# Kernel tuning notes

Measured on AMD Instinct MI355X. Metric: run time of the kernel, lower is better.

The kernel has to match this reference:

```python
import jax, jax.numpy as jnp
import numpy as np

B, T, E, H, D = 2, 2048, 1024, 16, 64
ROPE_BASE = 10000.0


def project(x, k):
    # Lift to Lorentz hyperboloid with curvature magnitude K=exp(k): <lx,lx>_L = -K
    K = jnp.exp(k)
    x0 = jnp.sqrt(K + jnp.sum(x * x, axis=-1, keepdims=True))
    return jnp.concatenate([x0, x], axis=-1)


def layer_norm(x, w, b, eps=1e-5):
    m = jnp.mean(x, axis=-1, keepdims=True)
    v = jnp.mean((x - m) ** 2, axis=-1, keepdims=True)
    return (x - m) * jax.lax.rsqrt(v + eps) * w + b


def setup_inputs() -> dict:
    key = jax.random.key(0)
    ks = jax.random.split(key, 8)
    s = 0.02
    return dict(
        x=jax.random.normal(ks[0], (B, T, E), jnp.float32),
        block_curvature=jnp.asarray(1.0, jnp.float32),
        mlp_curvature=jnp.asarray(1.0, jnp.float32),
        attn_curvatures=jnp.ones((1, H, 1, 1), jnp.float32),
        w_qkv=jax.random.normal(ks[1], (E + 1, 3 * E), jnp.float32) * s,
        w_attn_proj=jax.random.normal(ks[2], ((D + 1) * H, E), jnp.float32) * s,
        b_attn_proj=jnp.zeros((E,), jnp.float32),
        w_mlp_expand=jax.random.normal(ks[3], (E + 1, 4 * E + 3), jnp.float32) * s,
        b_mlp_expand=jnp.zeros((4 * E + 3,), jnp.float32),
        w_mlp_shrink=jax.random.normal(ks[4], (4 * (E + 1), E), jnp.float32) * s,
        b_mlp_shrink=jnp.zeros((E,), jnp.float32),
        ln_w=jnp.ones((E,), jnp.float32),
        ln_b=jnp.zeros((E,), jnp.float32),
    )


def _block(x, block_curvature, mlp_curvature, attn_curvatures, w_qkv,
           w_attn_proj, b_attn_proj, w_mlp_expand, b_mlp_expand,
           w_mlp_shrink, b_mlp_shrink, ln_w, ln_b):
    Bq, Tq = x.shape[0], x.shape[1]
    lx = project(x, block_curvature)  # (B,T,E+1)

    def block_norm(l):
        return project(layer_norm(l[..., 1:], ln_w, ln_b), block_curvature)

    def skip(l, f):  # hyperbolic skip: add space parts, re-lift
        return project(l[..., 1:] + f[..., 1:], block_curvature)

    def attn(l):
        qkv = l @ w_qkv  # (B,T,3E)
        q, k, v = jnp.split(qkv, 3, axis=-1)
        q = q.reshape(Bq, Tq, H, D)
        k = k.reshape(Bq, Tq, H, D)
        v = v.reshape(Bq, Tq, H, D)
        half = D // 2
        inv_freq = 1.0 / (ROPE_BASE ** (jnp.arange(0, D, 2, dtype=jnp.float32) / D))
        freqs = jnp.arange(Tq, dtype=jnp.float32)[:, None] * inv_freq[None, :]
        cos = jnp.cos(freqs)[None, :, None, :]  # (1,T,1,D/2)
        sin = jnp.sin(freqs)[None, :, None, :]

        def rope(t):
            t1, t2 = t[..., :half], t[..., half:]
            return jnp.concatenate([t1 * cos + t2 * sin, -t1 * sin + t2 * cos], axis=-1)

        q = rope(q).transpose(0, 2, 1, 3)  # (B,H,T,D)
        k = rope(k).transpose(0, 2, 1, 3)
        v = v.transpose(0, 2, 1, 3)
        K = jnp.exp(attn_curvatures)  # (1,H,1,1) per-head curvature
        qt = jnp.sqrt(K + jnp.sum(q * q, axis=-1, keepdims=True))  # time coord (B,H,T,1)
        kt = jnp.sqrt(K + jnp.sum(k * k, axis=-1, keepdims=True))
        lv = project(v, attn_curvatures)  # (B,H,T,D+1)
        # Lorentz inner product without materializing (B,H,T,T,D+1)
        inner = jnp.einsum('bhtd,bhsd->bhts', q, k) - qt * jnp.swapaxes(kt, -1, -2)
        ratio = jnp.maximum(-inner / K, 1.0 + 1e-7)
        dis = jnp.sqrt(K) * jnp.arccosh(ratio)  # (B,H,T,T)
        causal = jnp.tril(jnp.ones((Tq, Tq), dtype=bool))
        w = jnp.where(causal, -dis, -jnp.inf)  # neg_dis attention weight + causal bias
        aw = jax.nn.softmax(w, axis=-1)
        o = jnp.einsum('bhts,bhse->bhte', aw, lv)  # (B,H,T,D+1)
        lnorm2 = o[..., :1] ** 2 - jnp.sum(o[..., 1:] ** 2, axis=-1, keepdims=True)
        hn = jnp.sqrt(jnp.maximum(lnorm2, 1e-12))  # Lorentz norm
        o = o * jnp.sqrt(K) / hn  # renormalize back onto hyperboloid
        o = o.transpose(0, 2, 1, 3).reshape(Bq, Tq, H * (D + 1))
        return project(o @ w_attn_proj + b_attn_proj, block_curvature)

    def mlp(l):
        h = project(l @ w_mlp_expand + b_mlp_expand, mlp_curvature)[..., 1:]  # (B,T,4E+3)
        h = jax.nn.gelu(h, approximate=False)
        h = project(h, mlp_curvature)  # (B,T,4(E+1))
        return project(h @ w_mlp_shrink + b_mlp_shrink, block_curvature)

    lx = skip(lx, attn(block_norm(lx)))
    lx = skip(lx, mlp(block_norm(lx)))
    return lx


def reference(x, block_curvature, mlp_curvature, attn_curvatures, w_qkv,
              w_attn_proj, b_attn_proj, w_mlp_expand, b_mlp_expand,
              w_mlp_shrink, b_mlp_shrink, ln_w, ln_b):
    return _block(x, block_curvature, mlp_curvature, attn_curvatures, w_qkv,
                  w_attn_proj, b_attn_proj, w_mlp_expand, b_mlp_expand,
                  w_mlp_shrink, b_mlp_shrink, ln_w, ln_b)
```

## Files before the change

kernel.cpp:

```cpp
#include <hip/hip_runtime.h>
#include <math.h>

#define MM   4096
#define TT   2048
#define HH   16

typedef __bf16 bf16x8 __attribute__((ext_vector_type(8)));
typedef float f32x4 __attribute__((ext_vector_type(4)));

__device__ __forceinline__ void g2l16(const void* g, void* l) {
    __builtin_amdgcn_global_load_lds(
        (__attribute__((address_space(1))) void*)g,
        (__attribute__((address_space(3))) void*)l, 16, 0, 0);
}

#if __has_builtin(__builtin_amdgcn_exp2f)
__device__ __forceinline__ float fexp2(float x) { return __builtin_amdgcn_exp2f(x); }
#else
__device__ __forceinline__ float fexp2(float x) { return exp2f(x); }
#endif
#if __has_builtin(__builtin_amdgcn_logf)
__device__ __forceinline__ float flog2(float x) { return __builtin_amdgcn_logf(x); }
#else
__device__ __forceinline__ float flog2(float x) { return log2f(x); }
#endif
#if __has_builtin(__builtin_amdgcn_sqrtf)
__device__ __forceinline__ float fsqrt_(float x) { return __builtin_amdgcn_sqrtf(x); }
#else
__device__ __forceinline__ float fsqrt_(float x) { return sqrtf(x); }
#endif
#if __has_builtin(__builtin_amdgcn_rcpf)
__device__ __forceinline__ float frcp_(float x) { return __builtin_amdgcn_rcpf(x); }
#else
__device__ __forceinline__ float frcp_(float x) { return 1.0f / x; }
#endif
#if __has_builtin(__builtin_amdgcn_rsqf)
__device__ __forceinline__ float frsq_(float x) { return __builtin_amdgcn_rsqf(x); }
#else
__device__ __forceinline__ float frsq_(float x) { return rsqrtf(x); }
#endif

__device__ __forceinline__ float gelu_f(float x) {
    float u = 0.7978845608028654f * fmaf(0.044715f * x, x * x, x);
    u = fminf(fmaxf(u, -15.f), 15.f);
    float t = fexp2(-2.885390081777927f * u);
    return 0.5f * x * (1.f + (1.f - t) * frcp_(1.f + t));
}

__device__ __forceinline__ float blockSum256(float v, volatile float* sb) {
    int lane = threadIdx.x & 63, w = threadIdx.x >> 6;
#pragma unroll
    for (int o = 32; o; o >>= 1) v += __shfl_xor(v, o);
    if (lane == 0) sb[w] = v;
    __syncthreads();
    v = sb[0] + sb[1] + sb[2] + sb[3];
    __syncthreads();
    return v;
}

__global__ __launch_bounds__(256) void block_norm_bf_k(
    const float* __restrict__ in, int ld,
    __bf16* __restrict__ out, int ldo,
    const float* __restrict__ lw, const float* __restrict__ lb,
    const float* __restrict__ curv)
{
    int row = blockIdx.x;
    const float* x = in + (size_t)row * ld;
    __bf16* o = out + (size_t)row * ldo;
    __shared__ float sb[4];
    int tid = threadIdx.x;
    float v[4]; float s1 = 0.f, s2 = 0.f;
#pragma unroll
    for (int r = 0; r < 4; r++) {
        float t = x[tid + 256 * r];
        v[r] = t; s1 += t; s2 += t * t;
    }
    s1 = blockSum256(s1, sb);
    s2 = blockSum256(s2, sb);
    float mean = s1 * (1.f / 1024.f);
    float var  = s2 * (1.f / 1024.f) - mean * mean;
    float rs = rsqrtf(var + 1e-5f);
    float y[4]; float ssq = 0.f;
#pragma unroll
    for (int r = 0; r < 4; r++) {
        int i = tid + 256 * r;
        float t = (v[r] - mean) * rs * lw[i] + lb[i];
        y[r] = t; ssq += t * t;
    }
    ssq = blockSum256(ssq, sb);
#pragma unroll
    for (int r = 0; r < 4; r++) o[1 + tid + 256 * r] = (__bf16)y[r];
    if (tid == 0) o[0] = (__bf16)sqrtf(expf(*curv) + ssq);
    if (tid < ldo - 1025) o[1025 + tid] = (__bf16)0.f;
}

__global__ __launch_bounds__(256) void row_x0_k(
    float* __restrict__ buf, int stride, int n, const float* __restrict__ curv)
{
    int row = blockIdx.x;
    float* base = buf + (size_t)row * stride;
    __shared__ float sb[4];
    float s = 0.f;
    for (int i = threadIdx.x; i < n; i += 256) { float t = base[1 + i]; s += t * t; }
    s = blockSum256(s, sb);
    if (threadIdx.x == 0) base[0] = sqrtf(expf(*curv) + s);
}

__global__ __launch_bounds__(256) void row_x0_tail_k(
    __bf16* __restrict__ h,
    const __bf16* __restrict__ ln,
    const __bf16* __restrict__ Bt,
    const float* __restrict__ bias,
    const float* __restrict__ curv)
{
    int row = blockIdx.x;
    __bf16* base = h + (size_t)row * 4224;
    const __bf16* lnr = ln + (size_t)row * 1088;
    const __bf16* B0 = Bt + (size_t)4096 * 1088;
    const __bf16* B1 = Bt + (size_t)4097 * 1088;
    const __bf16* B2 = Bt + (size_t)4098 * 1088;
    __shared__ float sb[4];
    float d0 = 0.f, d1 = 0.f, d2 = 0.f;
    for (int i = threadIdx.x; i < 1088; i += 256) {
        float a = (float)lnr[i];
        d0 += a * (float)B0[i];
        d1 += a * (float)B1[i];
        d2 += a * (float)B2[i];
    }
    d0 = blockSum256(d0, sb);
    d1 = blockSum256(d1, sb);
    d2 = blockSum256(d2, sb);
    float t3[3] = {d0 + bias[4096], d1 + bias[4097], d2 + bias[4098]};
    float ssq_t = 0.f;
#pragma unroll
    for (int j = 0; j < 3; j++) {
        float v = gelu_f(t3[j]);
        t3[j] = v; ssq_t += v * v;
    }
    if (threadIdx.x == 0) {
        base[1 + 4096] = (__bf16)t3[0];
        base[1 + 4097] = (__bf16)t3[1];
        base[1 + 4098] = (__bf16)t3[2];
    }
    float s = 0.f;
    for (int i = threadIdx.x; i < 4096; i += 256) { float t = (float)base[1 + i]; s += t * t; }
    s = blockSum256(s, sb) + ssq_t;
    if (threadIdx.x == 0) base[0] = (__bf16)sqrtf(expf(*curv) + s);
    if (threadIdx.x < 124) base[4100 + threadIdx.x] = (__bf16)0.f;
}

__global__ __launch_bounds__(256) void wt_k(
    const float* __restrict__ W, int K, int N,
    __bf16* __restrict__ Wt, int Kp)
{
    __shared__ float s[32][33];
    int tx = threadIdx.x & 31, ty = threadIdx.x >> 5;
    int k0 = blockIdx.x * 32, n0 = blockIdx.y * 32;
#pragma unroll
    for (int r = 0; r < 4; r++) {
        int k = k0 + ty + 8 * r, n = n0 + tx;
        s[ty + 8 * r][tx] = (k < K && n < N) ? W[(size_t)k * N + n] : 0.f;
    }
    __syncthreads();
#pragma unroll
    for (int r = 0; r < 4; r++) {
        int n = n0 + ty + 8 * r, k = k0 + tx;
        if (n < N) Wt[(size_t)n * Kp + k] = (__bf16)s[tx][ty + 8 * r];
    }
}

template<bool BIAS, bool GELU, bool OUTBF>
__global__ __launch_bounds__(512, 2) void mgemm256_k(
    const __bf16* __restrict__ A, int lda,
    const __bf16* __restrict__ Bt, int ldb, int NB,
    const float* __restrict__ bias,
    void* __restrict__ Cout, int ldc,
    int N, int Kp)
{
    __shared__ __bf16 sAB[65536];
    const int tid = threadIdx.x;
    const int w = tid >> 6, lane = tid & 63;
    const int wm = w >> 2, wn = w & 3;
    const int lr = lane & 15, lq = lane >> 4;

    const int lin = blockIdx.y * gridDim.x + blockIdx.x;
    const int xcd = lin & 7, loc = lin >> 3;
    const int LN = gridDim.x >> 1, LM = gridDim.y >> 2;
    const int mt = (xcd >> 1) * LM + loc / LN;
    const int nt = (xcd & 1) * LN + loc % LN;
    const int m0 = mt * 256, n0 = nt * 256;

    const int rr  = tid >> 3;
    const int csw = ((tid & 7) ^ (rr & 7)) << 3;
    const __bf16* gA[4]; const __bf16* gB[4];
#pragma unroll
    for (int c = 0; c < 4; c++) {
        gA[c] = A + (size_t)(m0 + c * 64 + rr) * lda + csw;
        int rb = n0 + c * 64 + rr; rb = (rb < NB) ? rb : (NB - 1);
        gB[c] = Bt + (size_t)rb * ldb + csw;
    }
    __bf16* lA = sAB + (w << 9);
    __bf16* lB = sAB + 32768 + (w << 9);

    const int off0 = (lq * 8) ^ ((lr & 7) << 3);
    const int off1 = off0 ^ 32;
    const int arow = wm * 128 + lr;
    const int brow = wn * 64 + lr;

    f32x4 zero = {0.f, 0.f, 0.f, 0.f};
    f32x4 acc[8][4];
#pragma unroll
    for (int i = 0; i < 8; i++)
#pragma unroll
        for (int j = 0; j < 4; j++) acc[i][j] = zero;

#pragma unroll
    for (int c = 0; c < 4; c++) {
        g2l16(gA[c], lA + c * 4096);
        g2l16(gB[c], lB + c * 4096);
    }
    asm volatile("s_waitcnt vmcnt(0)" ::: "memory");
    __builtin_amdgcn_s_barrier();

    const int NT = Kp >> 6;
    for (int kt = 0; kt < NT; ++kt) {
        const int cur = kt & 1;
        const __bf16* pA = sAB + cur * 16384;
        const __bf16* pB = sAB + 32768 + cur * 16384;
        bf16x8 af[4][2], bfr[4][2];

        if (kt + 1 < NT) {
            const int ko = (kt + 1) << 6;
            __bf16* dA = lA + (cur ^ 1) * 16384;
            __bf16* dB = lB + (cur ^ 1) * 16384;
#pragma unroll
            for (int c = 0; c < 4; c++) {
                g2l16(gA[c] + ko, dA + c * 4096);
                g2l16(gB[c] + ko, dB + c * 4096);
            }
        }
#pragma unroll
        for (int i = 0; i < 4; i++) {
            const __bf16* r = pA + (arow + i * 16) * 64;
            af[i][0] = *(const bf16x8*)(r + off0);
            af[i][1] = *(const bf16x8*)(r + off1);
        }
#pragma unroll
        for (int j = 0; j < 2; j++) {
            const __bf16* r = pB + (brow + j * 16) * 64;
            bfr[j][0] = *(const bf16x8*)(r + off0);
            bfr[j][1] = *(const bf16x8*)(r + off1);
        }
        __builtin_amdgcn_s_barrier();
        __builtin_amdgcn_s_setprio(1);
#pragma unroll
        for (int ks = 0; ks < 2; ks++)
#pragma unroll
            for (int i = 0; i < 4; i++)
#pragma unroll
                for (int j = 0; j < 2; j++)
                    acc[i][j] = __builtin_amdgcn_mfma_f32_16x16x32_bf16(af[i][ks], bfr[j][ks], acc[i][j], 0, 0, 0);
        __builtin_amdgcn_s_setprio(0);
        __builtin_amdgcn_s_barrier();

#pragma unroll
        for (int j = 2; j < 4; j++) {
            const __bf16* r = pB + (brow + j * 16) * 64;
            bfr[j][0] = *(const bf16x8*)(r + off0);
            bfr[j][1] = *(const bf16x8*)(r + off1);
        }
        __builtin_amdgcn_s_barrier();
        __builtin_amdgcn_s_setprio(1);
#pragma unroll
        for (int ks = 0; ks < 2; ks++)
#pragma unroll
            for (int i = 0; i < 4; i++)
#pragma unroll
                for (int j = 2; j < 4; j++)
                    acc[i][j] = __builtin_amdgcn_mfma_f32_16x16x32_bf16(af[i][ks], bfr[j][ks], acc[i][j], 0, 0, 0);
        __builtin_amdgcn_s_setprio(0);
        __builtin_amdgcn_s_barrier();

#pragma unroll
        for (int i = 0; i < 4; i++) {
            const __bf16* r = pA + (arow + 64 + i * 16) * 64;
            af[i][0] = *(const bf16x8*)(r + off0);
            af[i][1] = *(const bf16x8*)(r + off1);
        }
        __builtin_amdgcn_s_barrier();
        __builtin_amdgcn_s_setprio(1);
#pragma unroll
        for (int ks = 0; ks < 2; ks++)
#pragma unroll
            for (int i = 0; i < 4; i++)
#pragma unroll
                for (int j = 0; j < 2; j++)
                    acc[4 + i][j] = __builtin_amdgcn_mfma_f32_16x16x32_bf16(af[i][ks], bfr[j][ks], acc[4 + i][j], 0, 0, 0);
        __builtin_amdgcn_s_setprio(0);
        __builtin_amdgcn_s_barrier();

        __builtin_amdgcn_s_setprio(1);
#pragma unroll
        for (int ks = 0; ks < 2; ks++)
#pragma unroll
            for (int i = 0; i < 4; i++)
#pragma unroll
                for (int j = 2; j < 4; j++)
                    acc[4 + i][j] = __builtin_amdgcn_mfma_f32_16x16x32_bf16(af[i][ks], bfr[j][ks], acc[4 + i][j], 0, 0, 0);
        __builtin_amdgcn_s_setprio(0);
        asm volatile("s_waitcnt vmcnt(0) lgkmcnt(0)" ::: "memory");
        __builtin_amdgcn_s_barrier();
    }

#pragma unroll
    for (int j = 0; j < 4; j++) {
        const int n = n0 + wn * 64 + j * 16 + lr;
        if (n < N) {
            const float bv = BIAS ? bias[n] : 0.f;
#pragma unroll
            for (int i = 0; i < 8; i++) {
#pragma unroll
                for (int r = 0; r < 4; r++) {
                    const int m = m0 + wm * 128 + i * 16 + lq * 4 + r;
                    float v = acc[i][j][r] + bv;
                    if (GELU) v = gelu_f(v);
                    if (OUTBF) ((__bf16*)Cout)[(size_t)m * ldc + n] = (__bf16)v;
                    else       ((float*)Cout)[(size_t)m * ldc + n] = v;
                }
            }
        }
    }
}

template<bool BIAS, bool GELU, bool SKIP>
__global__ __launch_bounds__(256, 2) void mgemm128_k(
    const __bf16* __restrict__ A, int lda,
    const __bf16* __restrict__ Bt, int ldb,
    const float* __restrict__ bias,
    const float* __restrict__ skip, int ldskip,
    float* __restrict__ Cout, int ldc,
    int N, int Kp)
{
    __shared__ __bf16 sAB[32768];
    const int tid = threadIdx.x;
    const int w = tid >> 6, lane = tid & 63;
    const int wm = w >> 1, wn = w & 1;
    const int lr = lane & 15, lq = lane >> 4;

    const int bid = blockIdx.x;
    const int cpx = gridDim.x >> 3;
    const int swz = (bid & 7) * cpx + (bid >> 3);
    const int m0 = (swz >> 3) * 128, n0 = (swz & 7) * 128;

    const int rr  = tid >> 3;
    const int csw = ((tid & 7) ^ (rr & 7)) << 3;
    const __bf16* gA[4]; const __bf16* gB[4];
#pragma unroll
    for (int c = 0; c < 4; c++) {
        gA[c] = A + (size_t)(m0 + c * 32 + rr) * lda + csw;
        gB[c] = Bt + (size_t)(n0 + c * 32 + rr) * ldb + csw;
    }
    __bf16* lA = sAB + (w << 9);
    __bf16* lB = sAB + 16384 + (w << 9);

    const int off0 = (lq * 8) ^ ((lr & 7) << 3);
    const int off1 = off0 ^ 32;
    const int arow = wm * 64 + lr;
    const int brow = wn * 64 + lr;

    f32x4 zero = {0.f, 0.f, 0.f, 0.f};
    f32x4 acc[4][4];
#pragma unroll
    for (int i = 0; i < 4; i++)
#pragma unroll
        for (int j = 0; j < 4; j++) acc[i][j] = zero;

#pragma unroll
    for (int c = 0; c < 4; c++) {
        g2l16(gA[c], lA + c * 2048);
        g2l16(gB[c], lB + c * 2048);
    }
    asm volatile("s_waitcnt vmcnt(0)" ::: "memory");
    __builtin_amdgcn_s_barrier();

    const int NT = Kp >> 6;
    for (int kt = 0; kt < NT; ++kt) {
        const int cur = kt & 1;
        const __bf16* pA = sAB + cur * 8192;
        const __bf16* pB = sAB + 16384 + cur * 8192;
        bf16x8 af[4][2], bfr[4][2];

        if (kt + 1 < NT) {
            const int ko = (kt + 1) << 6;
            __bf16* dA = lA + (cur ^ 1) * 8192;
            __bf16* dB = lB + (cur ^ 1) * 8192;
#pragma unroll
            for (int c = 0; c < 4; c++) {
                g2l16(gA[c] + ko, dA + c * 2048);
                g2l16(gB[c] + ko, dB + c * 2048);
            }
        }
#pragma unroll
        for (int i = 0; i < 4; i++) {
            const __bf16* r = pA + (arow + i * 16) * 64;
            af[i][0] = *(const bf16x8*)(r + off0);
            af[i][1] = *(const bf16x8*)(r + off1);
        }
#pragma unroll
        for (int j = 0; j < 2; j++) {
            const __bf16* r = pB + (brow + j * 16) * 64;
            bfr[j][0] = *(const bf16x8*)(r + off0);
            bfr[j][1] = *(const bf16x8*)(r + off1);
        }
        __builtin_amdgcn_s_barrier();
        __builtin_amdgcn_s_setprio(1);
#pragma unroll
        for (int ks = 0; ks < 2; ks++)
#pragma unroll
            for (int i = 0; i < 4; i++)
#pragma unroll
                for (int j = 0; j < 2; j++)
                    acc[i][j] = __builtin_amdgcn_mfma_f32_16x16x32_bf16(af[i][ks], bfr[j][ks], acc[i][j], 0, 0, 0);
        __builtin_amdgcn_s_setprio(0);
        __builtin_amdgcn_s_barrier();

#pragma unroll
        for (int j = 2; j < 4; j++) {
            const __bf16* r = pB + (brow + j * 16) * 64;
            bfr[j][0] = *(const bf16x8*)(r + off0);
            bfr[j][1] = *(const bf16x8*)(r + off1);
        }
        __builtin_amdgcn_s_barrier();
        __builtin_amdgcn_s_setprio(1);
#pragma unroll
        for (int ks = 0; ks < 2; ks++)
#pragma unroll
            for (int i = 0; i < 4; i++)
#pragma unroll
                for (int j = 2; j < 4; j++)
                    acc[i][j] = __builtin_amdgcn_mfma_f32_16x16x32_bf16(af[i][ks], bfr[j][ks], acc[i][j], 0, 0, 0);
        __builtin_amdgcn_s_setprio(0);
        asm volatile("s_waitcnt vmcnt(0) lgkmcnt(0)" ::: "memory");
        __builtin_amdgcn_s_barrier();
    }

#pragma unroll
    for (int j = 0; j < 4; j++) {
        const int n = n0 + wn * 64 + j * 16 + lr;
        if (n < N) {
            const float bv = BIAS ? bias[n] : 0.f;
#pragma unroll
            for (int i = 0; i < 4; i++) {
#pragma unroll
                for (int r = 0; r < 4; r++) {
                    const int m = m0 + wm * 64 + i * 16 + lq * 4 + r;
                    float v = acc[i][j][r] + bv;
                    if (GELU) v = gelu_f(v);
                    if (SKIP) v += skip[(size_t)m * ldskip + n];
                    Cout[(size_t)m * ldc + n] = v;
                }
            }
        }
    }
}

__global__ __launch_bounds__(256) void rope_k(
    float* __restrict__ QKV, const float* __restrict__ curv,
    float* __restrict__ qt, float* __restrict__ kt,
    __bf16* __restrict__ Kb, __bf16* __restrict__ Obf)
{
    int row = blockIdx.x;
    int b = row >> 11, t = row & (TT - 1);
    int wv = threadIdx.x >> 6, d = threadIdx.x & 63;
    int j = d & 31;
    float fr = (float)t * powf(10000.0f, -(float)(2 * j) / 64.0f);
    float cv = cosf(fr), sv = sinf(fr);
    float sgn = (d < 32) ? sv : -sv;
    for (int h = wv; h < HH; h += 4) {
        float Kh = expf(curv[h]);
        float* base = QKV + (size_t)row * 3072 + h * 64;
        float q = base[d], k = base[1024 + d];
        float qp = __shfl_xor(q, 32);
        float kp = __shfl_xor(k, 32);
        float qr = q * cv + qp * sgn;
        float kr = k * cv + kp * sgn;
        base[d] = qr;
        size_t oidx = ((size_t)(b * HH + h) * TT + t);
        Kb[oidx * 64 + d] = (__bf16)kr;
        float sq = qr * qr, sk = kr * kr;
#pragma unroll
        for (int o = 32; o; o >>= 1) {
            sq += __shfl_xor(sq, o);
            sk += __shfl_xor(sk, o);
        }
        if (d == 0) {
            qt[oidx] = sqrtf(Kh + sq);
            kt[oidx] = sqrtf(Kh + sk);
        }
    }
    if (threadIdx.x < 48) Obf[(size_t)row * 1088 + 1040 + threadIdx.x] = (__bf16)0.f;
}

__global__ __launch_bounds__(256) void vtrans_k(
    const float* __restrict__ QKV, const float* __restrict__ curv,
    __bf16* __restrict__ Vtb, float* __restrict__ vt)
{
    __shared__ float sT[64 * 65];
    int bh = blockIdx.y; int h = bh & (HH - 1); int b = bh >> 4;
    int t0 = blockIdx.x * 64;
    int tid = threadIdx.x, w = tid >> 6, lane = tid & 63;
    float Kh = expf(curv[h]);
    const float* vbase = QKV + (size_t)(b * TT + t0) * 3072 + 2048 + h * 64;
#pragma unroll 4
    for (int i = 0; i < 16; i++) {
        int tr = w * 16 + i;
        float v = vbase[(size_t)tr * 3072 + lane];
        sT[lane * 65 + tr] = v;
        float s = v * v;
#pragma unroll
        for (int o = 32; o; o >>= 1) s += __shfl_xor(s, o);
        if (lane == 0) vt[(size_t)bh * TT + t0 + tr] = sqrtf(Kh + s);
    }
    __syncthreads();
    int d = tid >> 2, seg = tid & 3;
    const float* r = &sT[d * 65 + seg * 16];
    bf16x8 o0, o1;
#pragma unroll
    for (int i = 0; i < 8; i++) { o0[i] = (__bf16)r[i]; o1[i] = (__bf16)r[8 + i]; }
    __bf16* dst = Vtb + ((size_t)bh * 64 + d) * TT + t0 + seg * 16;
    *(bf16x8*)dst = o0;
    *(bf16x8*)(dst + 8) = o1;
}

__global__ __launch_bounds__(256, 3) void flash_k(
    const float* __restrict__ QKV,
    const __bf16* __restrict__ Kb, const __bf16* __restrict__ Vtb,
    const float* __restrict__ qt, const float* __restrict__ kt,
    const float* __restrict__ vt,
    const float* __restrict__ curv,
    __bf16* __restrict__ O)
{
    __shared__ __bf16 sK[2][4096];
    __shared__ __bf16 sVt[2][4096];
    __shared__ __bf16 sP[4 * 16 * 72];
    __shared__ float skt[2][64], svt[2][64];

    int bh = blockIdx.x; int h = bh & (HH - 1); int b = bh >> 4;
    int qti = 31 - (int)blockIdx.y;
    int q0 = qti << 6;
    int NJ = qti + 1;
    float Kh = expf(curv[h]);
    float sqKh = sqrtf(Kh), msqK = -sqKh, invKh = 1.0f / Kh;
    const float* tok = QKV + (size_t)b * TT * 3072 + h * 64;
    const char* KbB = (const char*)Kb + (size_t)bh * TT * 128;
    const char* VtB = (const char*)Vtb + (size_t)bh * 64 * (TT * 2);
    const float* qtp = qt + (size_t)bh * TT;
    const float* ktp = kt + (size_t)bh * TT;
    const float* vtp = vt + (size_t)bh * TT;

    int tid = threadIdx.x;
    int w = tid >> 6, lane = tid & 63;
    int m = lane & 15, quad = lane >> 4;
    int myBase = q0 + 16 * w;
    __bf16* sPw = &sP[w * 16 * 72];

    bf16x8 qhi[2], qlo[2];
    {
        const float* qrow = tok + (size_t)(myBase + m) * 3072;
#pragma unroll
        for (int ks = 0; ks < 2; ks++) {
            const float* s = qrow + quad * 8 + 32 * ks;
            float4 f0 = *(const float4*)s;
            float4 f1 = *(const float4*)(s + 4);
            float fa[8] = {f0.x, f0.y, f0.z, f0.w, f1.x, f1.y, f1.z, f1.w};
#pragma unroll
            for (int jj = 0; jj < 8; jj++) {
                __bf16 hv = (__bf16)fa[jj];
                qhi[ks][jj] = hv;
                qlo[ks][jj] = (__bf16)(fa[jj] - (float)hv);
            }
        }
    }
    float qtv[4]; int qg[4];
#pragma unroll
    for (int r = 0; r < 4; r++) { qg[r] = myBase + quad * 4 + r; qtv[r] = qtp[qg[r]]; }

    f32x4 zero = {0.f, 0.f, 0.f, 0.f};
    f32x4 accO[4];
#pragma unroll
    for (int nt = 0; nt < 4; nt++) accO[nt] = zero;
    float lsumr[4] = {}, o0r[4] = {};

    {
        const char* kg = KbB + (size_t)lane * 128 + w * 16;
        char* sKb = (char*)&sK[0][0] + w * 1024;
        g2l16(kg,      sKb);
        g2l16(kg + 64, sKb + 4096);
        const char* vg = VtB + (size_t)lane * (TT * 2) + w * 16;
        char* sVb = (char*)&sVt[0][0] + w * 1024;
        g2l16(vg,      sVb);
        g2l16(vg + 64, sVb + 4096);
    }
    if (tid < 64) skt[0][tid] = ktp[tid];
    else if (tid < 128) svt[0][tid - 64] = vtp[tid - 64];
    __syncthreads();

    for (int j = 0; j < NJ; ++j) {
        int cur = j & 1;
        int sb = j << 6;
        if (j + 1 < NJ) {
            int sb2 = sb + 64;
            const char* kg = KbB + (size_t)(sb2 + lane) * 128 + w * 16;
            char* sKb = (char*)&sK[cur ^ 1][0] + w * 1024;
            g2l16(kg,      sKb);
            g2l16(kg + 64, sKb + 4096);
            const char* vg = VtB + (size_t)lane * (TT * 2) + sb2 * 2 + w * 16;
            char* sVb = (char*)&sVt[cur ^ 1][0] + w * 1024;
            g2l16(vg,      sVb);
            g2l16(vg + 64, sVb + 4096);
            if (tid < 64) skt[cur ^ 1][tid] = ktp[sb2 + tid];
            else if (tid < 128) svt[cur ^ 1][tid - 64] = vtp[sb2 + tid - 64];
        }

        f32x4 accS[4];
#pragma unroll
        for (int nt = 0; nt < 4; nt++) accS[nt] = zero;
#pragma unroll
        for (int nt = 0; nt < 4; nt++) {
#pragma unroll
            for (int ksp = 0; ksp < 2; ksp++) {
                bf16x8 bk = *(const bf16x8*)&sK[cur][((ksp * 4 + quad) * 64 + nt * 16 + m) * 8];
                accS[nt] = __builtin_amdgcn_mfma_f32_16x16x32_bf16(qhi[ksp], bk, accS[nt], 0, 0, 0);
                accS[nt] = __builtin_amdgcn_mfma_f32_16x16x32_bf16(qlo[ksp], bk, accS[nt], 0, 0, 0);
            }
        }
#pragma unroll
        for (int nt = 0; nt < 4; nt++) {
            int col = nt * 16 + m;
            int sglob = sb + col;
            float ktv = skt[cur][col], vtv = svt[cur][col];
#pragma unroll
            for (int r = 0; r < 4; r++) {
                float dot = accS[nt][r];
                float rdiff = fmaf(qtv[r], ktv, -dot);
                float ratio = fmaxf(rdiff * invKh, 1.0f + 1e-7f);
                float y = ratio + fsqrt_(fmaf(ratio, ratio, -1.0f));
                float pv = fexp2(msqK * flog2(y));
                float p = (sglob <= qg[r]) ? pv : 0.0f;
                lsumr[r] += p;
                o0r[r] = fmaf(p, vtv, o0r[r]);
                sPw[(quad * 4 + r) * 72 + col] = (__bf16)p;
            }
        }
        __asm__ volatile("s_waitcnt lgkmcnt(0)" ::: "memory");
#pragma unroll
        for (int ksp = 0; ksp < 2; ksp++) {
            bf16x8 aP = *(const bf16x8*)&sPw[m * 72 + ksp * 32 + quad * 8];
#pragma unroll
            for (int nt = 0; nt < 4; nt++) {
                bf16x8 bV = *(const bf16x8*)&sVt[cur][((ksp * 4 + quad) * 64 + nt * 16 + m) * 8];
                accO[nt] = __builtin_amdgcn_mfma_f32_16x16x32_bf16(aP, bV, accO[nt], 0, 0, 0);
            }
        }
        __syncthreads();
    }

#pragma unroll
    for (int r = 0; r < 4; r++) {
#pragma unroll
        for (int off = 1; off < 16; off <<= 1) {
            lsumr[r] += __shfl_xor(lsumr[r], off);
            o0r[r]   += __shfl_xor(o0r[r], off);
        }
    }
#pragma unroll
    for (int r = 0; r < 4; r++) {
        float inv = frcp_(lsumr[r]);
        float o0f = o0r[r] * inv;
        float ov[4]; float part = 0.f;
#pragma unroll
        for (int nt = 0; nt < 4; nt++) { float t = accO[nt][r] * inv; ov[nt] = t; part += t * t; }
        part += __shfl_xor(part, 1);
        part += __shfl_xor(part, 2);
        part += __shfl_xor(part, 4);
        part += __shfl_xor(part, 8);
        float scale = sqKh * frsq_(fmaxf(o0f * o0f - part, 1e-12f));
        size_t orow = (size_t)(b * TT + qg[r]) * 1088 + h * 65;
        if (m == 0) O[orow] = (__bf16)(o0f * scale);
#pragma unroll
        for (int nt = 0; nt < 4; nt++) O[orow + 1 + nt * 16 + m] = (__bf16)(ov[nt] * scale);
    }
}

extern "C" void kernel_launch(void* const* d_in, const int* in_sizes, int n_in,
                              void* d_out, int out_size, void* d_ws, size_t ws_size,
                              hipStream_t stream) {
    const float* x    = (const float*)d_in[0];
    const float* bc   = (const float*)d_in[1];
    const float* mc   = (const float*)d_in[2];
    const float* ac   = (const float*)d_in[3];
    const float* w_qkv = (const float*)d_in[4];
    const float* w_ap  = (const float*)d_in[5];
    const float* b_ap  = (const float*)d_in[6];
    const float* w_me  = (const float*)d_in[7];
    const float* b_me  = (const float*)d_in[8];
    const float* w_ms  = (const float*)d_in[9];
    const float* b_ms  = (const float*)d_in[10];
    const float* lnw  = (const float*)d_in[11];
    const float* lnb  = (const float*)d_in[12];
    float* out = (float*)d_out;
    float* ws  = (float*)d_ws;

    float* R      = ws;
    float* qkvbuf = R;
    float* X2     = R;
    __bf16* h_bf  = (__bf16*)(R + 4194304);
    float* p      = R + 12845056;
    __bf16* ln_bf = (__bf16*)p;  p += 2228224;
    __bf16* o_bf  = (__bf16*)p;  p += 2228224;
    __bf16* qkvT  = (__bf16*)p;  p += 1671168;
    __bf16* apT   = (__bf16*)p;  p += 557056;
    float*  meT_f = p;           p += 2229856;
    float*  msT_f = p;           p += 2162688;
    float* Qt = p;               p += 2 * HH * TT;
    float* Kt = p;               p += 2 * HH * TT;
    float* Vt = p;
    __bf16* meT = (__bf16*)meT_f;
    __bf16* msT = (__bf16*)msT_f;
    __bf16* Kb  = (__bf16*)meT_f;
    __bf16* Vtb = (__bf16*)msT_f;

    wt_k<<<dim3(34, 96),  256, 0, stream>>>(w_qkv, 1025, 3072, qkvT, 1088);
    wt_k<<<dim3(34, 32),  256, 0, stream>>>(w_ap,  1040, 1024, apT,  1088);

    block_norm_bf_k<<<MM, 256, 0, stream>>>(x, 1024, ln_bf, 1088, lnw, lnb, bc);
    mgemm256_k<false, false, false><<<dim3(12, 16), 512, 0, stream>>>(
        ln_bf, 1088, qkvT, 1088, 3072, nullptr, qkvbuf, 3072, 3072, 1088);
    rope_k<<<MM, 256, 0, stream>>>(qkvbuf, ac, Qt, Kt, Kb, o_bf);
    vtrans_k<<<dim3(32, 32), 256, 0, stream>>>(qkvbuf, ac, Vtb, Vt);
    flash_k<<<dim3(2 * HH, 32), 256, 0, stream>>>(qkvbuf, Kb, Vtb, Qt, Kt, Vt, ac, o_bf);
    wt_k<<<dim3(34, 129), 256, 0, stream>>>(w_me,  1025, 4099, meT, 1088);
    wt_k<<<dim3(132, 32), 256, 0, stream>>>(w_ms,  4100, 1024, msT, 4224);
    mgemm128_k<true, false, true><<<dim3(256), 256, 0, stream>>>(
        o_bf, 1088, apT, 1088, b_ap, x, 1024, X2, 1024, 1024, 1088);
    block_norm_bf_k<<<MM, 256, 0, stream>>>(X2, 1024, ln_bf, 1088, lnw, lnb, bc);
    mgemm256_k<true, true, true><<<dim3(16, 16), 512, 0, stream>>>(
        ln_bf, 1088, meT, 1088, 4099, b_me, (void*)(h_bf + 1), 4224, 4099, 1088);
    row_x0_tail_k<<<MM, 256, 0, stream>>>(h_bf, ln_bf, meT, b_me, mc);
    mgemm128_k<true, false, true><<<dim3(256), 256, 0, stream>>>(
        h_bf, 4224, msT, 4224, b_ms, X2, 1024, out + 1, 1025, 1024, 4224);
    row_x0_k<<<MM, 256, 0, stream>>>(out, 1025, 1024, bc);
}
```

Baseline: 444.4 us.

## Enlarge flash query tile to 128 rows and use 128-tile GEMM for QKV

The flash attention kernel now runs 8 waves per block over 128 query rows, up from 4 waves over 64. Each K/V tile loaded into LDS is therefore reused by twice as many query rows, and each thread issues one async load per tile. MFMA sections are wrapped in s_setprio so matrix work gets issue priority over the softmax ALU code. The QKV projection moves from the 256-tile GEMM to the 128-tile GEMM, which gains a configurable N-tile count, to launch more blocks. The risks are more register and LDS pressure per block and coarser causal work balance across blocks.

```diff
diff --git a/kernel.cpp b/kernel.cpp
--- a/kernel.cpp
+++ b/kernel.cpp
@@ -339,7 +339,7 @@
     const float* __restrict__ bias,
     const float* __restrict__ skip, int ldskip,
     float* __restrict__ Cout, int ldc,
-    int N, int Kp)
+    int N, int Kp, int nT)
 {
     __shared__ __bf16 sAB[32768];
     const int tid = threadIdx.x;
@@ -350,7 +350,7 @@
     const int bid = blockIdx.x;
     const int cpx = gridDim.x >> 3;
     const int swz = (bid & 7) * cpx + (bid >> 3);
-    const int m0 = (swz >> 3) * 128, n0 = (swz & 7) * 128;
+    const int m0 = (swz / nT) * 128, n0 = (swz % nT) * 128;
 
     const int rr  = tid >> 3;
     const int csw = ((tid & 7) ^ (rr & 7)) << 3;
@@ -532,7 +532,7 @@
     *(bf16x8*)(dst + 8) = o1;
 }
 
-__global__ __launch_bounds__(256, 3) void flash_k(
+__global__ __launch_bounds__(512, 4) void flash_k(
     const float* __restrict__ QKV,
     const __bf16* __restrict__ Kb, const __bf16* __restrict__ Vtb,
     const float* __restrict__ qt, const float* __restrict__ kt,
@@ -542,13 +542,13 @@
 {
     __shared__ __bf16 sK[2][4096];
     __shared__ __bf16 sVt[2][4096];
-    __shared__ __bf16 sP[4 * 16 * 72];
+    __shared__ __bf16 sP[8 * 16 * 72];
     __shared__ float skt[2][64], svt[2][64];
 
     int bh = blockIdx.x; int h = bh & (HH - 1); int b = bh >> 4;
-    int qti = 31 - (int)blockIdx.y;
-    int q0 = qti << 6;
-    int NJ = qti + 1;
+    int qti = 15 - (int)blockIdx.y;
+    int q0 = qti << 7;
+    int NJ = (qti << 1) + 2;
     float Kh = expf(curv[h]);
     float sqKh = sqrtf(Kh), msqK = -sqKh, invKh = 1.0f / Kh;
     const float* tok = QKV + (size_t)b * TT * 3072 + h * 64;
@@ -561,6 +561,7 @@
     int tid = threadIdx.x;
     int w = tid >> 6, lane = tid & 63;
     int m = lane & 15, quad = lane >> 4;
+    int wq = w & 3, half = w >> 2;
     int myBase = q0 + 16 * w;
     __bf16* sPw = &sP[w * 16 * 72];
 
@@ -591,16 +592,10 @@
     for (int nt = 0; nt < 4; nt++) accO[nt] = zero;
     float lsumr[4] = {}, o0r[4] = {};
 
-    {
-        const char* kg = KbB + (size_t)lane * 128 + w * 16;
-        char* sKb = (char*)&sK[0][0] + w * 1024;
-        g2l16(kg,      sKb);
-        g2l16(kg + 64, sKb + 4096);
-        const char* vg = VtB + (size_t)lane * (TT * 2) + w * 16;
-        char* sVb = (char*)&sVt[0][0] + w * 1024;
-        g2l16(vg,      sVb);
-        g2l16(vg + 64, sVb + 4096);
-    }
+    const int stoff = half * 4096 + wq * 1024;
+
+    g2l16(KbB + (size_t)lane * 128 + half * 64 + wq * 16, (char*)&sK[0][0] + stoff);
+    g2l16(VtB + (size_t)lane * (TT * 2) + half * 64 + wq * 16, (char*)&sVt[0][0] + stoff);
     if (tid < 64) skt[0][tid] = ktp[tid];
     else if (tid < 128) svt[0][tid - 64] = vtp[tid - 64];
     __syncthreads();
@@ -610,14 +605,10 @@
         int sb = j << 6;
         if (j + 1 < NJ) {
             int sb2 = sb + 64;
-            const char* kg = KbB + (size_t)(sb2 + lane) * 128 + w * 16;
-            char* sKb = (char*)&sK[cur ^ 1][0] + w * 1024;
-            g2l16(kg,      sKb);
-            g2l16(kg + 64, sKb + 4096);
-            const char* vg = VtB + (size_t)lane * (TT * 2) + sb2 * 2 + w * 16;
-            char* sVb = (char*)&sVt[cur ^ 1][0] + w * 1024;
-            g2l16(vg,      sVb);
-            g2l16(vg + 64, sVb + 4096);
+            g2l16(KbB + (size_t)(sb2 + lane) * 128 + half * 64 + wq * 16,
+                  (char*)&sK[cur ^ 1][0] + stoff);
+            g2l16(VtB + (size_t)lane * (TT * 2) + sb2 * 2 + half * 64 + wq * 16,
+                  (char*)&sVt[cur ^ 1][0] + stoff);
             if (tid < 64) skt[cur ^ 1][tid] = ktp[sb2 + tid];
             else if (tid < 128) svt[cur ^ 1][tid - 64] = vtp[sb2 + tid - 64];
         }
@@ -625,6 +616,7 @@
         f32x4 accS[4];
 #pragma unroll
         for (int nt = 0; nt < 4; nt++) accS[nt] = zero;
+        __builtin_amdgcn_s_setprio(1);
 #pragma unroll
         for (int nt = 0; nt < 4; nt++) {
 #pragma unroll
@@ -634,6 +626,7 @@
                 accS[nt] = __builtin_amdgcn_mfma_f32_16x16x32_bf16(qlo[ksp], bk, accS[nt], 0, 0, 0);
             }
         }
+        __builtin_amdgcn_s_setprio(0);
 #pragma unroll
         for (int nt = 0; nt < 4; nt++) {
             int col = nt * 16 + m;
@@ -653,6 +646,7 @@
             }
         }
         __asm__ volatile("s_waitcnt lgkmcnt(0)" ::: "memory");
+        __builtin_amdgcn_s_setprio(1);
 #pragma unroll
         for (int ksp = 0; ksp < 2; ksp++) {
             bf16x8 aP = *(const bf16x8*)&sPw[m * 72 + ksp * 32 + quad * 8];
@@ -662,6 +656,7 @@
                 accO[nt] = __builtin_amdgcn_mfma_f32_16x16x32_bf16(aP, bV, accO[nt], 0, 0, 0);
             }
         }
+        __builtin_amdgcn_s_setprio(0);
         __syncthreads();
     }
 
@@ -734,20 +729,20 @@
     wt_k<<<dim3(34, 32),  256, 0, stream>>>(w_ap,  1040, 1024, apT,  1088);
 
     block_norm_bf_k<<<MM, 256, 0, stream>>>(x, 1024, ln_bf, 1088, lnw, lnb, bc);
-    mgemm256_k<false, false, false><<<dim3(12, 16), 512, 0, stream>>>(
-        ln_bf, 1088, qkvT, 1088, 3072, nullptr, qkvbuf, 3072, 3072, 1088);
+    mgemm128_k<false, false, false><<<dim3(768), 256, 0, stream>>>(
+        ln_bf, 1088, qkvT, 1088, nullptr, nullptr, 0, qkvbuf, 3072, 3072, 1088, 24);
     rope_k<<<MM, 256, 0, stream>>>(qkvbuf, ac, Qt, Kt, Kb, o_bf);
     vtrans_k<<<dim3(32, 32), 256, 0, stream>>>(qkvbuf, ac, Vtb, Vt);
-    flash_k<<<dim3(2 * HH, 32), 256, 0, stream>>>(qkvbuf, Kb, Vtb, Qt, Kt, Vt, ac, o_bf);
+    flash_k<<<dim3(2 * HH, 16), 512, 0, stream>>>(qkvbuf, Kb, Vtb, Qt, Kt, Vt, ac, o_bf);
     wt_k<<<dim3(34, 129), 256, 0, stream>>>(w_me,  1025, 4099, meT, 1088);
     wt_k<<<dim3(132, 32), 256, 0, stream>>>(w_ms,  4100, 1024, msT, 4224);
     mgemm128_k<true, false, true><<<dim3(256), 256, 0, stream>>>(
-        o_bf, 1088, apT, 1088, b_ap, x, 1024, X2, 1024, 1024, 1088);
+        o_bf, 1088, apT, 1088, b_ap, x, 1024, X2, 1024, 1024, 1088, 8);
     block_norm_bf_k<<<MM, 256, 0, stream>>>(X2, 1024, ln_bf, 1088, lnw, lnb, bc);
     mgemm256_k<true, true, true><<<dim3(16, 16), 512, 0, stream>>>(
         ln_bf, 1088, meT, 1088, 4099, b_me, (void*)(h_bf + 1), 4224, 4099, 1088);
     row_x0_tail_k<<<MM, 256, 0, stream>>>(h_bf, ln_bf, meT, b_me, mc);
     mgemm128_k<true, false, true><<<dim3(256), 256, 0, stream>>>(
-        h_bf, 4224, msT, 4224, b_ms, X2, 1024, out + 1, 1025, 1024, 4224);
+        h_bf, 4224, msT, 4224, b_ms, X2, 1024, out + 1, 1025, 1024, 4224, 8);
     row_x0_k<<<MM, 256, 0, stream>>>(out, 1025, 1024, bc);
 }
```

After: 463.3 us. +4.2%, slower.

## Replace 256-tile GEMM with a 3-stage, BK=32, 128-tile GEMM for all projections

Applied to the files above, without the earlier changes.

Drops the 512-thread 256x256 GEMM kernel and routes the QKV and MLP-expand GEMMs through a reworked 128x128 kernel. That kernel now uses a K-step of 32, a three-buffer global-to-LDS pipeline with partial vmcnt waits, a new swizzle, and launch bounds of 3 blocks per CU. A bf16-output template flag is added so it can also serve the expand GEMM. The aim is more blocks in flight and deeper prefetch, traded against lower per-tile data reuse. The expand GEMM now computes only 4096 columns, which relies on the tail kernel covering the remaining ones.

```diff
diff --git a/kernel.cpp b/kernel.cpp
--- a/kernel.cpp
+++ b/kernel.cpp
@@ -169,179 +169,16 @@
     }
 }
 
-template<bool BIAS, bool GELU, bool OUTBF>
-__global__ __launch_bounds__(512, 2) void mgemm256_k(
-    const __bf16* __restrict__ A, int lda,
-    const __bf16* __restrict__ Bt, int ldb, int NB,
-    const float* __restrict__ bias,
-    void* __restrict__ Cout, int ldc,
-    int N, int Kp)
-{
-    __shared__ __bf16 sAB[65536];
-    const int tid = threadIdx.x;
-    const int w = tid >> 6, lane = tid & 63;
-    const int wm = w >> 2, wn = w & 3;
-    const int lr = lane & 15, lq = lane >> 4;
-
-    const int lin = blockIdx.y * gridDim.x + blockIdx.x;
-    const int xcd = lin & 7, loc = lin >> 3;
-    const int LN = gridDim.x >> 1, LM = gridDim.y >> 2;
-    const int mt = (xcd >> 1) * LM + loc / LN;
-    const int nt = (xcd & 1) * LN + loc % LN;
-    const int m0 = mt * 256, n0 = nt * 256;
-
-    const int rr  = tid >> 3;
-    const int csw = ((tid & 7) ^ (rr & 7)) << 3;
-    const __bf16* gA[4]; const __bf16* gB[4];
-#pragma unroll
-    for (int c = 0; c < 4; c++) {
-        gA[c] = A + (size_t)(m0 + c * 64 + rr) * lda + csw;
-        int rb = n0 + c * 64 + rr; rb = (rb < NB) ? rb : (NB - 1);
-        gB[c] = Bt + (size_t)rb * ldb + csw;
-    }
-    __bf16* lA = sAB + (w << 9);
-    __bf16* lB = sAB + 32768 + (w << 9);
-
-    const int off0 = (lq * 8) ^ ((lr & 7) << 3);
-    const int off1 = off0 ^ 32;
-    const int arow = wm * 128 + lr;
-    const int brow = wn * 64 + lr;
-
-    f32x4 zero = {0.f, 0.f, 0.f, 0.f};
-    f32x4 acc[8][4];
-#pragma unroll
-    for (int i = 0; i < 8; i++)
-#pragma unroll
-        for (int j = 0; j < 4; j++) acc[i][j] = zero;
-
-#pragma unroll
-    for (int c = 0; c < 4; c++) {
-        g2l16(gA[c], lA + c * 4096);
-        g2l16(gB[c], lB + c * 4096);
-    }
-    asm volatile("s_waitcnt vmcnt(0)" ::: "memory");
-    __builtin_amdgcn_s_barrier();
-
-    const int NT = Kp >> 6;
-    for (int kt = 0; kt < NT; ++kt) {
-        const int cur = kt & 1;
-        const __bf16* pA = sAB + cur * 16384;
-        const __bf16* pB = sAB + 32768 + cur * 16384;
-        bf16x8 af[4][2], bfr[4][2];
-
-        if (kt + 1 < NT) {
-            const int ko = (kt + 1) << 6;
-            __bf16* dA = lA + (cur ^ 1) * 16384;
-            __bf16* dB = lB + (cur ^ 1) * 16384;
-#pragma unroll
-            for (int c = 0; c < 4; c++) {
-                g2l16(gA[c] + ko, dA + c * 4096);
-                g2l16(gB[c] + ko, dB + c * 4096);
-            }
-        }
-#pragma unroll
-        for (int i = 0; i < 4; i++) {
-            const __bf16* r = pA + (arow + i * 16) * 64;
-            af[i][0] = *(const bf16x8*)(r + off0);
-            af[i][1] = *(const bf16x8*)(r + off1);
-        }
-#pragma unroll
-        for (int j = 0; j < 2; j++) {
-            const __bf16* r = pB + (brow + j * 16) * 64;
-            bfr[j][0] = *(const bf16x8*)(r + off0);
-            bfr[j][1] = *(const bf16x8*)(r + off1);
-        }
-        __builtin_amdgcn_s_barrier();
-        __builtin_amdgcn_s_setprio(1);
-#pragma unroll
-        for (int ks = 0; ks < 2; ks++)
-#pragma unroll
-            for (int i = 0; i < 4; i++)
-#pragma unroll
-                for (int j = 0; j < 2; j++)
-                    acc[i][j] = __builtin_amdgcn_mfma_f32_16x16x32_bf16(af[i][ks], bfr[j][ks], acc[i][j], 0, 0, 0);
-        __builtin_amdgcn_s_setprio(0);
-        __builtin_amdgcn_s_barrier();
-
-#pragma unroll
-        for (int j = 2; j < 4; j++) {
-            const __bf16* r = pB + (brow + j * 16) * 64;
-            bfr[j][0] = *(const bf16x8*)(r + off0);
-            bfr[j][1] = *(const bf16x8*)(r + off1);
-        }
-        __builtin_amdgcn_s_barrier();
-        __builtin_amdgcn_s_setprio(1);
-#pragma unroll
-        for (int ks = 0; ks < 2; ks++)
-#pragma unroll
-            for (int i = 0; i < 4; i++)
-#pragma unroll
-                for (int j = 2; j < 4; j++)
-                    acc[i][j] = __builtin_amdgcn_mfma_f32_16x16x32_bf16(af[i][ks], bfr[j][ks], acc[i][j], 0, 0, 0);
-        __builtin_amdgcn_s_setprio(0);
-        __builtin_amdgcn_s_barrier();
-
-#pragma unroll
-        for (int i = 0; i < 4; i++) {
-            const __bf16* r = pA + (arow + 64 + i * 16) * 64;
-            af[i][0] = *(const bf16x8*)(r + off0);
-            af[i][1] = *(const bf16x8*)(r + off1);
-        }
-        __builtin_amdgcn_s_barrier();
-        __builtin_amdgcn_s_setprio(1);
-#pragma unroll
-        for (int ks = 0; ks < 2; ks++)
-#pragma unroll
-            for (int i = 0; i < 4; i++)
-#pragma unroll
-                for (int j = 0; j < 2; j++)
-                    acc[4 + i][j] = __builtin_amdgcn_mfma_f32_16x16x32_bf16(af[i][ks], bfr[j][ks], acc[4 + i][j], 0, 0, 0);
-        __builtin_amdgcn_s_setprio(0);
-        __builtin_amdgcn_s_barrier();
-
-        __builtin_amdgcn_s_setprio(1);
-#pragma unroll
-        for (int ks = 0; ks < 2; ks++)
-#pragma unroll
-            for (int i = 0; i < 4; i++)
-#pragma unroll
-                for (int j = 2; j < 4; j++)
-                    acc[4 + i][j] = __builtin_amdgcn_mfma_f32_16x16x32_bf16(af[i][ks], bfr[j][ks], acc[4 + i][j], 0, 0, 0);
-        __builtin_amdgcn_s_setprio(0);
-        asm volatile("s_waitcnt vmcnt(0) lgkmcnt(0)" ::: "memory");
-        __builtin_amdgcn_s_barrier();
-    }
-
-#pragma unroll
-    for (int j = 0; j < 4; j++) {
-        const int n = n0 + wn * 64 + j * 16 + lr;
-        if (n < N) {
-            const float bv = BIAS ? bias[n] : 0.f;
-#pragma unroll
-            for (int i = 0; i < 8; i++) {
-#pragma unroll
-                for (int r = 0; r < 4; r++) {
-                    const int m = m0 + wm * 128 + i * 16 + lq * 4 + r;
-                    float v = acc[i][j][r] + bv;
-                    if (GELU) v = gelu_f(v);
-                    if (OUTBF) ((__bf16*)Cout)[(size_t)m * ldc + n] = (__bf16)v;
-                    else       ((float*)Cout)[(size_t)m * ldc + n] = v;
-                }
-            }
-        }
-    }
-}
-
-template<bool BIAS, bool GELU, bool SKIP>
-__global__ __launch_bounds__(256, 2) void mgemm128_k(
+template<bool BIAS, bool GELU, bool SKIP, bool OUTBF>
+__global__ __launch_bounds__(256, 3) void mgemm128_k(
     const __bf16* __restrict__ A, int lda,
     const __bf16* __restrict__ Bt, int ldb,
     const float* __restrict__ bias,
     const float* __restrict__ skip, int ldskip,
-    float* __restrict__ Cout, int ldc,
-    int N, int Kp)
-{
-    __shared__ __bf16 sAB[32768];
+    void* __restrict__ Cout, int ldc,
+    int N, int Kp, int nT)
+{
+    __shared__ __bf16 sAB[24576];
     const int tid = threadIdx.x;
     const int w = tid >> 6, lane = tid & 63;
     const int wm = w >> 1, wn = w & 1;
@@ -350,21 +187,19 @@
     const int bid = blockIdx.x;
     const int cpx = gridDim.x >> 3;
     const int swz = (bid & 7) * cpx + (bid >> 3);
-    const int m0 = (swz >> 3) * 128, n0 = (swz & 7) * 128;
-
-    const int rr  = tid >> 3;
-    const int csw = ((tid & 7) ^ (rr & 7)) << 3;
-    const __bf16* gA[4]; const __bf16* gB[4];
-#pragma unroll
-    for (int c = 0; c < 4; c++) {
-        gA[c] = A + (size_t)(m0 + c * 32 + rr) * lda + csw;
-        gB[c] = Bt + (size_t)(n0 + c * 32 + rr) * ldb + csw;
-    }
-    __bf16* lA = sAB + (w << 9);
-    __bf16* lB = sAB + 16384 + (w << 9);
-
-    const int off0 = (lq * 8) ^ ((lr & 7) << 3);
-    const int off1 = off0 ^ 32;
+    const int m0 = (swz / nT) * 128, n0 = (swz % nT) * 128;
+
+    const int rr  = tid >> 2;
+    const int csw = ((tid & 3) ^ ((rr >> 1) & 3)) << 3;
+    const __bf16* gA[2]; const __bf16* gB[2];
+#pragma unroll
+    for (int c = 0; c < 2; c++) {
+        gA[c] = A + (size_t)(m0 + c * 64 + rr) * lda + csw;
+        gB[c] = Bt + (size_t)(n0 + c * 64 + rr) * ldb + csw;
+    }
+    const int wst = w * 512;
+
+    const int off = (lq ^ ((lr >> 1) & 3)) << 3;
     const int arow = wm * 64 + lr;
     const int brow = wn * 64 + lr;
 
@@ -375,73 +210,49 @@
 #pragma unroll
         for (int j = 0; j < 4; j++) acc[i][j] = zero;
 
-#pragma unroll
-    for (int c = 0; c < 4; c++) {
-        g2l16(gA[c], lA + c * 2048);
-        g2l16(gB[c], lB + c * 2048);
-    }
-    asm volatile("s_waitcnt vmcnt(0)" ::: "memory");
+    const int NT = Kp >> 5;
+#pragma unroll
+    for (int c = 0; c < 2; c++) {
+        g2l16(gA[c], sAB + c * 2048 + wst);
+        g2l16(gB[c], sAB + 12288 + c * 2048 + wst);
+    }
+#pragma unroll
+    for (int c = 0; c < 2; c++) {
+        g2l16(gA[c] + 32, sAB + 4096 + c * 2048 + wst);
+        g2l16(gB[c] + 32, sAB + 12288 + 4096 + c * 2048 + wst);
+    }
+    asm volatile("s_waitcnt vmcnt(4)" ::: "memory");
     __builtin_amdgcn_s_barrier();
 
-    const int NT = Kp >> 6;
+    int cur = 0;
     for (int kt = 0; kt < NT; ++kt) {
-        const int cur = kt & 1;
-        const __bf16* pA = sAB + cur * 8192;
-        const __bf16* pB = sAB + 16384 + cur * 8192;
-        bf16x8 af[4][2], bfr[4][2];
-
-        if (kt + 1 < NT) {
-            const int ko = (kt + 1) << 6;
-            __bf16* dA = lA + (cur ^ 1) * 8192;
-            __bf16* dB = lB + (cur ^ 1) * 8192;
-#pragma unroll
-            for (int c = 0; c < 4; c++) {
-                g2l16(gA[c] + ko, dA + c * 2048);
-                g2l16(gB[c] + ko, dB + c * 2048);
+        if (kt + 2 < NT) {
+            const int sbuf = (cur == 0) ? 2 : (cur - 1);
+            const int ko = (kt + 2) << 5;
+#pragma unroll
+            for (int c = 0; c < 2; c++) {
+                g2l16(gA[c] + ko, sAB + sbuf * 4096 + c * 2048 + wst);
+                g2l16(gB[c] + ko, sAB + 12288 + sbuf * 4096 + c * 2048 + wst);
             }
         }
-#pragma unroll
-        for (int i = 0; i < 4; i++) {
-            const __bf16* r = pA + (arow + i * 16) * 64;
-            af[i][0] = *(const bf16x8*)(r + off0);
-            af[i][1] = *(const bf16x8*)(r + off1);
-        }
-#pragma unroll
-        for (int j = 0; j < 2; j++) {
-            const __bf16* r = pB + (brow + j * 16) * 64;
-            bfr[j][0] = *(const bf16x8*)(r + off0);
-            bfr[j][1] = *(const bf16x8*)(r + off1);
-        }
+        const __bf16* pA = sAB + cur * 4096;
+        const __bf16* pB = sAB + 12288 + cur * 4096;
+        bf16x8 af[4], bf[4];
+#pragma unroll
+        for (int i = 0; i < 4; i++) af[i] = *(const bf16x8*)&pA[(arow + i * 16) * 32 + off];
+#pragma unroll
+        for (int j = 0; j < 4; j++) bf[j] = *(const bf16x8*)&pB[(brow + j * 16) * 32 + off];
+        __builtin_amdgcn_s_setprio(1);
+#pragma unroll
+        for (int i = 0; i < 4; i++)
+#pragma unroll
+            for (int j = 0; j < 4; j++)
+                acc[i][j] = __builtin_amdgcn_mfma_f32_16x16x32_bf16(af[i], bf[j], acc[i][j], 0, 0, 0);
+        __builtin_amdgcn_s_setprio(0);
+        if (kt + 2 < NT) { asm volatile("s_waitcnt vmcnt(4)" ::: "memory"); }
+        else             { asm volatile("s_waitcnt vmcnt(0) lgkmcnt(0)" ::: "memory"); }
         __builtin_amdgcn_s_barrier();
-        __builtin_amdgcn_s_setprio(1);
-#pragma unroll
-        for (int ks = 0; ks < 2; ks++)
-#pragma unroll
-            for (int i = 0; i < 4; i++)
-#pragma unroll
-                for (int j = 0; j < 2; j++)
-                    acc[i][j] = __builtin_amdgcn_mfma_f32_16x16x32_bf16(af[i][ks], bfr[j][ks], acc[i][j], 0, 0, 0);
-        __builtin_amdgcn_s_setprio(0);
-        __builtin_amdgcn_s_barrier();
-
-#pragma unroll
-        for (int j = 2; j < 4; j++) {
-            const __bf16* r = pB + (brow + j * 16) * 64;
-            bfr[j][0] = *(const bf16x8*)(r + off0);
-            bfr[j][1] = *(const bf16x8*)(r + off1);
-        }
-        __builtin_amdgcn_s_barrier();
-        __builtin_amdgcn_s_setprio(1);
-#pragma unroll
-        for (int ks = 0; ks < 2; ks++)
-#pragma unroll
-            for (int i = 0; i < 4; i++)
-#pragma unroll
-                for (int j = 2; j < 4; j++)
-                    acc[i][j] = __builtin_amdgcn_mfma_f32_16x16x32_bf16(af[i][ks], bfr[j][ks], acc[i][j], 0, 0, 0);
-        __builtin_amdgcn_s_setprio(0);
-        asm volatile("s_waitcnt vmcnt(0) lgkmcnt(0)" ::: "memory");
-        __builtin_amdgcn_s_barrier();
+        cur = (cur == 2) ? 0 : (cur + 1);
     }
 
 #pragma unroll
@@ -457,7 +268,8 @@
                     float v = acc[i][j][r] + bv;
                     if (GELU) v = gelu_f(v);
                     if (SKIP) v += skip[(size_t)m * ldskip + n];
-                    Cout[(size_t)m * ldc + n] = v;
+                    if (OUTBF) ((__bf16*)Cout)[(size_t)m * ldc + n] = (__bf16)v;
+                    else       ((float*)Cout)[(size_t)m * ldc + n] = v;
                 }
             }
         }
@@ -734,20 +546,20 @@
     wt_k<<<dim3(34, 32),  256, 0, stream>>>(w_ap,  1040, 1024, apT,  1088);
 
     block_norm_bf_k<<<MM, 256, 0, stream>>>(x, 1024, ln_bf, 1088, lnw, lnb, bc);
-    mgemm256_k<false, false, false><<<dim3(12, 16), 512, 0, stream>>>(
-        ln_bf, 1088, qkvT, 1088, 3072, nullptr, qkvbuf, 3072, 3072, 1088);
+    mgemm128_k<false, false, false, false><<<dim3(768), 256, 0, stream>>>(
+        ln_bf, 1088, qkvT, 1088, nullptr, nullptr, 0, qkvbuf, 3072, 3072, 1088, 24);
     rope_k<<<MM, 256, 0, stream>>>(qkvbuf, ac, Qt, Kt, Kb, o_bf);
     vtrans_k<<<dim3(32, 32), 256, 0, stream>>>(qkvbuf, ac, Vtb, Vt);
     flash_k<<<dim3(2 * HH, 32), 256, 0, stream>>>(qkvbuf, Kb, Vtb, Qt, Kt, Vt, ac, o_bf);
     wt_k<<<dim3(34, 129), 256, 0, stream>>>(w_me,  1025, 4099, meT, 1088);
     wt_k<<<dim3(132, 32), 256, 0, stream>>>(w_ms,  4100, 1024, msT, 4224);
-    mgemm128_k<true, false, true><<<dim3(256), 256, 0, stream>>>(
-        o_bf, 1088, apT, 1088, b_ap, x, 1024, X2, 1024, 1024, 1088);
+    mgemm128_k<true, false, true, false><<<dim3(256), 256, 0, stream>>>(
+        o_bf, 1088, apT, 1088, b_ap, x, 1024, X2, 1024, 1024, 1088, 8);
     block_norm_bf_k<<<MM, 256, 0, stream>>>(X2, 1024, ln_bf, 1088, lnw, lnb, bc);
-    mgemm256_k<true, true, true><<<dim3(16, 16), 512, 0, stream>>>(
-        ln_bf, 1088, meT, 1088, 4099, b_me, (void*)(h_bf + 1), 4224, 4099, 1088);
+    mgemm128_k<true, true, false, true><<<dim3(1024), 256, 0, stream>>>(
+        ln_bf, 1088, meT, 1088, b_me, nullptr, 0, (void*)(h_bf + 1), 4224, 4096, 1088, 32);
     row_x0_tail_k<<<MM, 256, 0, stream>>>(h_bf, ln_bf, meT, b_me, mc);
-    mgemm128_k<true, false, true><<<dim3(256), 256, 0, stream>>>(
-        h_bf, 4224, msT, 4224, b_ms, X2, 1024, out + 1, 1025, 1024, 4224);
+    mgemm128_k<true, false, true, false><<<dim3(256), 256, 0, stream>>>(
+        h_bf, 4224, msT, 4224, b_ms, X2, 1024, (void*)(out + 1), 1025, 1024, 4224, 8);
     row_x0_k<<<MM, 256, 0, stream>>>(out, 1025, 1024, bc);
 }
```

New measurement: 457.4 us. 2.9% more time.
